# Kernel tuning notes

Hardware: AMD Instinct MI355X
Metric: run time of the kernel (lower is better)

Reference implementation:

```python
import jax, jax.numpy as jnp
import numpy as np


def setup_inputs() -> dict:
    key = jax.random.key(0)
    k1, k2, k3, k4 = jax.random.split(key, 4)
    B, C = 32768, 10
    x = jax.random.normal(k1, (B, 1, 28, 28), dtype=jnp.float32)
    linear_weight = jax.random.normal(k2, (4 * 14 * 14 + 1 + 2, C), dtype=jnp.float32)
    linear_bias = jax.random.normal(k3, (C,), dtype=jnp.float32)
    sampler_weights = jax.random.normal(k4, (4,), dtype=jnp.float32)
    return {"x": x, "linear_weight": linear_weight, "linear_bias": linear_bias,
            "sampler_weights": sampler_weights}


def reference(x, linear_weight, linear_bias, sampler_weights):
    # Closed-form simulation of the 4-qubit circuits:
    # RY(t)|0> -> <Z>=cos(t); after CX(0,1): <Z1> = cos(t0)*cos(t1); CX(2,3) likewise.
    B = x.shape[0]
    # Extract non-overlapping 2x2 patches in row-major order -> (B, 196, 4)
    p = x[:, 0].reshape(B, 14, 2, 14, 2).transpose(0, 1, 3, 2, 4).reshape(B, 196, 4)
    c = jnp.cos(p)
    # quanvolution_circuit per patch: [cos a, cos a cos b, cos c, cos c cos d]
    feats = jnp.stack([c[..., 0], c[..., 0] * c[..., 1],
                       c[..., 2], c[..., 2] * c[..., 3]], axis=-1)  # (B,196,4)
    qfeat = feats.reshape(B, 784)
    # fully_connected_circuit on qfeat[:, :4]: mean of the four post-CX <Z>
    cf = jnp.cos(qfeat[:, :4])
    qfc = (cf[:, 0] + cf[:, 0] * cf[:, 1] + cf[:, 2] + cf[:, 2] * cf[:, 3]) / 4.0  # (B,)
    # sampler_circuit: sequential RY angles add on wires 0 and 1
    t0 = qfeat[:, 0] + sampler_weights[0] + sampler_weights[2]
    t1 = qfeat[:, 1] + sampler_weights[1] + sampler_weights[3]
    z0 = jnp.cos(t0)
    z1 = z0 * jnp.cos(t1)
    sampler = jax.nn.softmax(jnp.stack([z0, z1], axis=-1), axis=-1)  # (B,2)
    combined = jnp.concatenate([qfeat, qfc[:, None], sampler], axis=-1)  # (B,787)
    logits = combined @ linear_weight + linear_bias
    return jax.nn.log_softmax(logits, axis=-1)
```

## Files before the change

### kernel.cpp

```cpp
#include <hip/hip_runtime.h>


__global__ __launch_bounds__(256, 5)
void qml_k1(const float* __restrict__ x,
            const float* __restrict__ wm,
            float* __restrict__ part,
            float* __restrict__ qf,
            int B, int nblk)
{
    __shared__ float lds[64 * 128];

    const int t = threadIdx.x;
    const int lane = t & 63;
    const int wv = __builtin_amdgcn_readfirstlane((int)(t >> 6));
    const int g = blockIdx.x;
    const int ps = blockIdx.y;

    {
        const int base_s = g * 64;
#pragma unroll
        for (int k = 0; k < 7; ++k) {
            const int f = k * 256 + t;
            const int s = f / 28;
            const int c = f - 28 * s;
            int sg = base_s + s; if (sg >= B) sg = B - 1;
            const float4 v = *(const float4*)(x + (size_t)sg * 784 + ps * 112 + 4 * c);
            const int m2 = (s & 15) << 1;
            float* __restrict__ d0 = lds + s * 128 + ((4 * c) ^ m2);
            float* __restrict__ d1 = lds + s * 128 + ((4 * c + 2) ^ m2);
            *(float2*)d0 = make_float2(v.x, v.y);
            *(float2*)d1 = make_float2(v.z, v.w);
        }
    }
    __syncthreads();

    const int i_loc = wv >> 1;
    const int jbase = 7 * (wv & 1);
    const int o_top = i_loc * 56 + 2 * jbase;
    const int p0 = (2 * ps + i_loc) * 14 + jbase;
    const int m2 = (lane & 15) << 1;
    const float* __restrict__ row = lds + lane * 128;

    float acc[10];
#pragma unroll
    for (int c = 0; c < 10; ++c) acc[c] = 0.0f;
    float q0 = 0.f, q1 = 0.f, q2 = 0.f, q3 = 0.f;

#pragma unroll
    for (int tt = 0; tt < 7; ++tt) {
        const int ot = o_top + 2 * tt;
        const float2 a = *(const float2*)(row + (ot ^ m2));
        const float2 b = *(const float2*)(row + ((ot + 28) ^ m2));

        const float c0 = __cosf(a.x);
        const float c1 = __cosf(a.y);
        const float c2 = __cosf(b.x);
        const float c3 = __cosf(b.y);
        const float v0 = c0, v1 = c0 * c1, v2 = c2, v3 = c2 * c3;

        if (ps == 0 && wv == 0 && tt == 0) { q0 = v0; q1 = v1; q2 = v2; q3 = v3; }

        const float* __restrict__ wr = wm + 40 * (p0 + tt);
#pragma unroll
        for (int c = 0; c < 10; ++c)
            acc[c] += v0 * wr[c] + v1 * wr[10 + c] + v2 * wr[20 + c] + v3 * wr[30 + c];
    }

    __syncthreads();

    if (wv != 0) {
#pragma unroll
        for (int c = 0; c < 10; ++c) lds[(wv - 1) * 704 + lane * 11 + c] = acc[c];
    }
    __syncthreads();

    if (wv == 0) {
#pragma unroll
        for (int c = 0; c < 10; ++c)
            acc[c] += lds[lane * 11 + c] + lds[704 + lane * 11 + c]
                    + lds[1408 + lane * 11 + c];

        float* __restrict__ dst = part + (size_t)(ps * nblk + g) * 640;
#pragma unroll
        for (int c = 0; c < 10; ++c) dst[c * 64 + lane] = acc[c];

        if (ps == 0) {
            const int sample = g * 64 + lane;
            if (sample < B) {
                qf[0 * (size_t)B + sample] = q0;
                qf[1 * (size_t)B + sample] = q1;
                qf[2 * (size_t)B + sample] = q2;
                qf[3 * (size_t)B + sample] = q3;
            }
        }
    }
}

__global__ __launch_bounds__(640, 1)
void qml_k2(const float* __restrict__ part,
            const float* __restrict__ qf,
            const float* __restrict__ wm,
            const float* __restrict__ bias,
            const float* __restrict__ sw,
            float* __restrict__ out,
            int B, int nblk)
{
    __shared__ float lg[64 * 11];

    const int t = threadIdx.x;
    const int g = blockIdx.x;
    const int c = t >> 6;
    const int s = t & 63;

    float sum = 0.0f;
#pragma unroll
    for (int ps = 0; ps < 7; ++ps)
        sum += part[(size_t)(ps * nblk + g) * 640 + c * 64 + s];

    int sample = g * 64 + s;
    const bool ok = (sample < B);
    if (sample >= B) sample = B - 1;

    const float q0 = qf[0 * (size_t)B + sample];
    const float q1 = qf[1 * (size_t)B + sample];
    const float q2 = qf[2 * (size_t)B + sample];
    const float q3 = qf[3 * (size_t)B + sample];

    const float f0 = __cosf(q0), f1 = __cosf(q1);
    const float f2 = __cosf(q2), f3 = __cosf(q3);
    const float qfc = (f0 + f0 * f1 + f2 + f2 * f3) * 0.25f;

    const float t0 = q0 + sw[0] + sw[2];
    const float t1 = q1 + sw[1] + sw[3];
    const float z0 = __cosf(t0);
    const float z1 = z0 * __cosf(t1);
    const float e0 = __expf(z0);
    const float e1 = __expf(z1);
    const float inv = 1.0f / (e0 + e1);
    const float s0 = e0 * inv, s1 = e1 * inv;

    const float* __restrict__ wt = wm + 7840;
    const float logit = sum + bias[c] + qfc * wt[c] + s0 * wt[10 + c] + s1 * wt[20 + c];
    lg[s * 11 + c] = logit;
    __syncthreads();

    const int s2 = t / 10;
    const int c2 = t - 10 * s2;
    float m = -3.4e38f;
#pragma unroll
    for (int k = 0; k < 10; ++k) m = fmaxf(m, lg[s2 * 11 + k]);
    float ssum = 0.0f;
#pragma unroll
    for (int k = 0; k < 10; ++k) ssum += __expf(lg[s2 * 11 + k] - m);
    const float lse = __logf(ssum) + m;

    if (g * 64 + s2 < B)
        out[(size_t)g * 640 + t] = lg[s2 * 11 + c2] - lse;
}

extern "C" void kernel_launch(void* const* d_in, const int* in_sizes, int n_in,
                              void* d_out, int out_size, void* d_ws, size_t ws_size,
                              hipStream_t stream) {
    const float* x    = (const float*)d_in[0];
    const float* w    = (const float*)d_in[1];
    const float* bias = (const float*)d_in[2];
    const float* sw   = (const float*)d_in[3];
    float* out = (float*)d_out;

    const int B = in_sizes[0] / 784;
    const int nblk = (B + 63) / 64;

    float* part = (float*)d_ws;
    float* qf   = part + (size_t)7 * nblk * 640;

    dim3 grid1(nblk, 7);
    qml_k1<<<grid1, 256, 0, stream>>>(x, w, part, qf, B, nblk);
    qml_k2<<<nblk, 640, 0, stream>>>(part, qf, w, bias, sw, out, B, nblk);
}
```

Measured before the change: 165.0 us.

## Fuse partial-sum and logsoftmax kernels into one double-buffered per-block kernel

Replaces the two-kernel scheme (7-way split over patch rows writing partial logits, then a reduction/log-softmax kernel) with a single kernel where each block handles all 7 row strips for 64 samples. Row strips are double-buffered in LDS with register prefetch of the next strip while computing the current one. This removes the partial-sum workspace traffic and the second launch, but reduces grid parallelism to one block per 64 samples and uses larger LDS, lowering occupancy.

```diff
diff --git a/kernel.cpp b/kernel.cpp
--- a/kernel.cpp
+++ b/kernel.cpp
@@ -1,161 +1,150 @@
 #include <hip/hip_runtime.h>
 
 
-__global__ __launch_bounds__(256, 5)
-void qml_k1(const float* __restrict__ x,
-            const float* __restrict__ wm,
-            float* __restrict__ part,
-            float* __restrict__ qf,
-            int B, int nblk)
+#define ROWF 128
+
+__global__ __launch_bounds__(256, 2)
+void qml_fused(const float* __restrict__ x,
+               const float* __restrict__ wm,
+               const float* __restrict__ bias,
+               const float* __restrict__ sw,
+               float* __restrict__ out,
+               int B)
 {
-    __shared__ float lds[64 * 128];
+    __shared__ float lds[2][64 * ROWF];
 
     const int t = threadIdx.x;
     const int lane = t & 63;
     const int wv = __builtin_amdgcn_readfirstlane((int)(t >> 6));
     const int g = blockIdx.x;
-    const int ps = blockIdx.y;
 
-    {
-        const int base_s = g * 64;
+    int sample = g * 64 + lane;
+    const bool s_ok = (sample < B);
+    if (sample >= B) sample = B - 1;
+
+    const float* xb[7];
+    int d0[7], d1[7];
 #pragma unroll
-        for (int k = 0; k < 7; ++k) {
-            const int f = k * 256 + t;
-            const int s = f / 28;
-            const int c = f - 28 * s;
-            int sg = base_s + s; if (sg >= B) sg = B - 1;
-            const float4 v = *(const float4*)(x + (size_t)sg * 784 + ps * 112 + 4 * c);
-            const int m2 = (s & 15) << 1;
-            float* __restrict__ d0 = lds + s * 128 + ((4 * c) ^ m2);
-            float* __restrict__ d1 = lds + s * 128 + ((4 * c + 2) ^ m2);
-            *(float2*)d0 = make_float2(v.x, v.y);
-            *(float2*)d1 = make_float2(v.z, v.w);
-        }
+    for (int k = 0; k < 7; ++k) {
+        const int f = k * 256 + t;
+        const int s = f / 28;
+        const int c = f - 28 * s;
+        int sg = g * 64 + s; if (sg >= B) sg = B - 1;
+        xb[k] = x + (size_t)sg * 784 + 4 * c;
+        const int m2 = (s & 15) << 1;
+        d0[k] = s * ROWF + ((4 * c) ^ m2);
+        d1[k] = s * ROWF + ((4 * c + 2) ^ m2);
     }
-    __syncthreads();
 
     const int i_loc = wv >> 1;
     const int jbase = 7 * (wv & 1);
     const int o_top = i_loc * 56 + 2 * jbase;
-    const int p0 = (2 * ps + i_loc) * 14 + jbase;
-    const int m2 = (lane & 15) << 1;
-    const float* __restrict__ row = lds + lane * 128;
+    const int m2c = (lane & 15) << 1;
 
     float acc[10];
 #pragma unroll
     for (int c = 0; c < 10; ++c) acc[c] = 0.0f;
     float q0 = 0.f, q1 = 0.f, q2 = 0.f, q3 = 0.f;
 
+    float4 pre[7];
+
 #pragma unroll
-    for (int tt = 0; tt < 7; ++tt) {
-        const int ot = o_top + 2 * tt;
-        const float2 a = *(const float2*)(row + (ot ^ m2));
-        const float2 b = *(const float2*)(row + ((ot + 28) ^ m2));
+    for (int k = 0; k < 7; ++k) pre[k] = *(const float4*)(xb[k]);
+#pragma unroll
+    for (int k = 0; k < 7; ++k) {
+        *(float2*)(&lds[0][0] + d0[k]) = make_float2(pre[k].x, pre[k].y);
+        *(float2*)(&lds[0][0] + d1[k]) = make_float2(pre[k].z, pre[k].w);
+    }
+    __syncthreads();
 
-        const float c0 = __cosf(a.x);
-        const float c1 = __cosf(a.y);
-        const float c2 = __cosf(b.x);
-        const float c3 = __cosf(b.y);
-        const float v0 = c0, v1 = c0 * c1, v2 = c2, v3 = c2 * c3;
+#pragma unroll
+    for (int ps = 0; ps < 7; ++ps) {
+        const int cur = ps & 1, nxt = cur ^ 1;
 
-        if (ps == 0 && wv == 0 && tt == 0) { q0 = v0; q1 = v1; q2 = v2; q3 = v3; }
+        if (ps < 6) {
+#pragma unroll
+            for (int k = 0; k < 7; ++k)
+                pre[k] = *(const float4*)(xb[k] + (ps + 1) * 112);
+        }
 
-        const float* __restrict__ wr = wm + 40 * (p0 + tt);
+        const float* __restrict__ row = &lds[cur][0] + lane * ROWF;
+        const int p0 = (2 * ps + i_loc) * 14 + jbase;
+
 #pragma unroll
-        for (int c = 0; c < 10; ++c)
-            acc[c] += v0 * wr[c] + v1 * wr[10 + c] + v2 * wr[20 + c] + v3 * wr[30 + c];
+        for (int tt = 0; tt < 7; ++tt) {
+            const int ot = o_top + 2 * tt;
+            const float2 a = *(const float2*)(row + (ot ^ m2c));
+            const float2 b = *(const float2*)(row + ((ot + 28) ^ m2c));
+
+            const float c0 = __cosf(a.x);
+            const float c1 = __cosf(a.y);
+            const float c2 = __cosf(b.x);
+            const float c3 = __cosf(b.y);
+            const float v0 = c0, v1 = c0 * c1, v2 = c2, v3 = c2 * c3;
+
+            if (ps == 0 && wv == 0 && tt == 0) { q0 = v0; q1 = v1; q2 = v2; q3 = v3; }
+
+            const float* __restrict__ wr = wm + 40 * (p0 + tt);
+#pragma unroll
+            for (int c = 0; c < 10; ++c)
+                acc[c] += v0 * wr[c] + v1 * wr[10 + c] + v2 * wr[20 + c] + v3 * wr[30 + c];
+        }
+
+        if (ps < 6) {
+#pragma unroll
+            for (int k = 0; k < 7; ++k) {
+                *(float2*)(&lds[nxt][0] + d0[k]) = make_float2(pre[k].x, pre[k].y);
+                *(float2*)(&lds[nxt][0] + d1[k]) = make_float2(pre[k].z, pre[k].w);
+            }
+        }
+        __syncthreads();
     }
 
-    __syncthreads();
-
+    float* __restrict__ red = &lds[0][0];
     if (wv != 0) {
 #pragma unroll
-        for (int c = 0; c < 10; ++c) lds[(wv - 1) * 704 + lane * 11 + c] = acc[c];
+        for (int c = 0; c < 10; ++c) red[(wv - 1) * 704 + lane * 11 + c] = acc[c];
     }
     __syncthreads();
 
     if (wv == 0) {
 #pragma unroll
         for (int c = 0; c < 10; ++c)
-            acc[c] += lds[lane * 11 + c] + lds[704 + lane * 11 + c]
-                    + lds[1408 + lane * 11 + c];
+            acc[c] += red[lane * 11 + c] + red[704 + lane * 11 + c]
+                    + red[1408 + lane * 11 + c];
 
-        float* __restrict__ dst = part + (size_t)(ps * nblk + g) * 640;
+        const float f0 = __cosf(q0), f1 = __cosf(q1);
+        const float f2 = __cosf(q2), f3 = __cosf(q3);
+        const float qfc = (f0 + f0 * f1 + f2 + f2 * f3) * 0.25f;
+
+        const float t0 = q0 + sw[0] + sw[2];
+        const float t1 = q1 + sw[1] + sw[3];
+        const float z0 = __cosf(t0);
+        const float z1 = z0 * __cosf(t1);
+        const float e0 = __expf(z0);
+        const float e1 = __expf(z1);
+        const float inv = 1.0f / (e0 + e1);
+        const float s0 = e0 * inv, s1 = e1 * inv;
+
+        const float* __restrict__ wt = wm + 7840;
 #pragma unroll
-        for (int c = 0; c < 10; ++c) dst[c * 64 + lane] = acc[c];
+        for (int c = 0; c < 10; ++c)
+            acc[c] += qfc * wt[c] + s0 * wt[10 + c] + s1 * wt[20 + c] + bias[c];
 
-        if (ps == 0) {
-            const int sample = g * 64 + lane;
-            if (sample < B) {
-                qf[0 * (size_t)B + sample] = q0;
-                qf[1 * (size_t)B + sample] = q1;
-                qf[2 * (size_t)B + sample] = q2;
-                qf[3 * (size_t)B + sample] = q3;
-            }
+        float m = acc[0];
+#pragma unroll
+        for (int c = 1; c < 10; ++c) m = fmaxf(m, acc[c]);
+        float ssum = 0.0f;
+#pragma unroll
+        for (int c = 0; c < 10; ++c) ssum += __expf(acc[c] - m);
+        const float lse = __logf(ssum) + m;
+
+        if (s_ok) {
+            float* __restrict__ orow = out + (size_t)sample * 10;
+#pragma unroll
+            for (int c = 0; c < 10; ++c) orow[c] = acc[c] - lse;
         }
     }
-}
-
-__global__ __launch_bounds__(640, 1)
-void qml_k2(const float* __restrict__ part,
-            const float* __restrict__ qf,
-            const float* __restrict__ wm,
-            const float* __restrict__ bias,
-            const float* __restrict__ sw,
-            float* __restrict__ out,
-            int B, int nblk)
-{
-    __shared__ float lg[64 * 11];
-
-    const int t = threadIdx.x;
-    const int g = blockIdx.x;
-    const int c = t >> 6;
-    const int s = t & 63;
-
-    float sum = 0.0f;
-#pragma unroll
-    for (int ps = 0; ps < 7; ++ps)
-        sum += part[(size_t)(ps * nblk + g) * 640 + c * 64 + s];
-
-    int sample = g * 64 + s;
-    const bool ok = (sample < B);
-    if (sample >= B) sample = B - 1;
-
-    const float q0 = qf[0 * (size_t)B + sample];
-    const float q1 = qf[1 * (size_t)B + sample];
-    const float q2 = qf[2 * (size_t)B + sample];
-    const float q3 = qf[3 * (size_t)B + sample];
-
-    const float f0 = __cosf(q0), f1 = __cosf(q1);
-    const float f2 = __cosf(q2), f3 = __cosf(q3);
-    const float qfc = (f0 + f0 * f1 + f2 + f2 * f3) * 0.25f;
-
-    const float t0 = q0 + sw[0] + sw[2];
-    const float t1 = q1 + sw[1] + sw[3];
-    const float z0 = __cosf(t0);
-    const float z1 = z0 * __cosf(t1);
-    const float e0 = __expf(z0);
-    const float e1 = __expf(z1);
-    const float inv = 1.0f / (e0 + e1);
-    const float s0 = e0 * inv, s1 = e1 * inv;
-
-    const float* __restrict__ wt = wm + 7840;
-    const float logit = sum + bias[c] + qfc * wt[c] + s0 * wt[10 + c] + s1 * wt[20 + c];
-    lg[s * 11 + c] = logit;
-    __syncthreads();
-
-    const int s2 = t / 10;
-    const int c2 = t - 10 * s2;
-    float m = -3.4e38f;
-#pragma unroll
-    for (int k = 0; k < 10; ++k) m = fmaxf(m, lg[s2 * 11 + k]);
-    float ssum = 0.0f;
-#pragma unroll
-    for (int k = 0; k < 10; ++k) ssum += __expf(lg[s2 * 11 + k] - m);
-    const float lse = __logf(ssum) + m;
-
-    if (g * 64 + s2 < B)
-        out[(size_t)g * 640 + t] = lg[s2 * 11 + c2] - lse;
 }
 
 extern "C" void kernel_launch(void* const* d_in, const int* in_sizes, int n_in,
@@ -169,11 +158,5 @@
 
     const int B = in_sizes[0] / 784;
     const int nblk = (B + 63) / 64;
-
-    float* part = (float*)d_ws;
-    float* qf   = part + (size_t)7 * nblk * 640;
-
-    dim3 grid1(nblk, 7);
-    qml_k1<<<grid1, 256, 0, stream>>>(x, w, part, qf, B, nblk);
-    qml_k2<<<nblk, 640, 0, stream>>>(part, qf, w, bias, sw, out, B, nblk);
+    qml_fused<<<nblk, 256, 0, stream>>>(x, w, bias, sw, out, B);
 }
```

Result: slower. 173.1 us (+4.9%).
